# Kernel tuning notes

Hardware: AMD Instinct MI355X
Metric: run time of the kernel (lower is better)

The kernel has to match this reference:

```python
import jax, jax.numpy as jnp
import numpy as np

B, L, D, V, K = 4, 2048, 1024, 32, 4096  # batch, seq, embedding_dim, vq_dim, num_embeddings


def setup_inputs() -> dict:
    key = jax.random.key(0)
    k0, k1, k2, k3 = jax.random.split(key, 4)
    h = jax.random.normal(k0, (B, L, D), jnp.float32)
    attn_mask = jnp.ones((B, L), jnp.float32)
    # proj: Linear(D -> V); proj_inv: Linear(V -> D)
    Wp = jax.random.normal(k1, (V, D), jnp.float32) / np.float32(np.sqrt(D))
    bp = jnp.zeros((V,), jnp.float32)
    Wpi = jax.random.normal(k2, (D, V), jnp.float32) / np.float32(np.sqrt(V))
    bpi = jnp.zeros((D,), jnp.float32)
    # embedding init uniform(-1/K, 1/K)
    emb = jax.random.uniform(k3, (K, V), jnp.float32, -1.0 / K, 1.0 / K)
    return {"h": h, "attn_mask": attn_mask, "Wp": Wp, "bp": bp,
            "Wpi": Wpi, "bpi": bpi, "emb": emb}


def reference(h, attn_mask, Wp, bp, Wpi, bpi, emb, temperature=1.0):
    # project + L2 normalize
    hp = jnp.einsum('bld,vd->blv', h, Wp) + bp            # [B,L,V]
    hp = hp / jnp.linalg.norm(hp, axis=-1, keepdims=True)
    # normalize codebook (in torch this is an in-place .data update)
    emb_n = emb / jnp.linalg.norm(emb, axis=-1, keepdims=True)  # [K,V]
    # squared euclidean distances hp vs codebook
    d = (jnp.sum(hp * hp, axis=-1, keepdims=True)
         + jnp.sum(emb_n * emb_n, axis=-1)
         - 2.0 * jnp.einsum('blv,kv->blk', hp, emb_n))    # [B,L,K]
    A = jax.nn.softmax(-d / temperature, axis=-1)         # [B,L,K]
    code = jnp.argmax(A, axis=-1)                         # [B,L]
    h_vq = jnp.einsum('blk,kv->blv', A, emb_n)            # train mode: A @ embedding
    # masked scatter into zeros is equivalent to masking out unselected positions
    m = (attn_mask == 1)
    quantized = jnp.where(m[..., None], h_vq, jnp.float32(0.0))
    vq_code = jnp.where(m, code, 0).astype(jnp.int32)
    quantized = jnp.einsum('blv,dv->bld', quantized, Wpi) + bpi
    vq_loss = jnp.float32(0.0)
    return quantized, vq_code, vq_loss
```

## Files before the change

kernel.cpp:

```cpp
#include <hip/hip_runtime.h>
#include <hip/hip_bf16.h>
#include <math.h>

#define NTOK 8192
#define DIM  1024
#define VDIM 32
#define KCODES 4096

#define SC 2.8853900817779268f

typedef __attribute__((ext_vector_type(8))) short short8;
typedef __attribute__((ext_vector_type(4))) float f32x4;

#define MFMA16(A,B,C) __builtin_amdgcn_mfma_f32_16x16x32_bf16(A, B, C, 0, 0, 0)

__device__ __forceinline__ unsigned short f2bf(float x) {
    unsigned u = __builtin_bit_cast(unsigned, x);
    u += 0x7FFF + ((u >> 16) & 1);
    return (unsigned short)(u >> 16);
}
__device__ __forceinline__ float bf2f(unsigned short b) {
    unsigned u = ((unsigned)b) << 16;
    return __builtin_bit_cast(float, u);
}
__device__ __forceinline__ float fexp2(float x) {
#if __has_builtin(__builtin_amdgcn_exp2f)
    return __builtin_amdgcn_exp2f(x);
#else
    return __expf(0.6931471805599453f * x);
#endif
}

struct U4 { unsigned x, y, z, w; };

__device__ __forceinline__ void split8(const float* p, short8* H, short8* L) {
    unsigned hh[4], ll[4];
    #pragma unroll
    for (int i = 0; i < 4; ++i) {
        unsigned short a = f2bf(p[2 * i]);
        unsigned short b = f2bf(p[2 * i + 1]);
        hh[i] = (unsigned)a | ((unsigned)b << 16);
        unsigned short la = f2bf(p[2 * i] - bf2f(a));
        unsigned short lb = f2bf(p[2 * i + 1] - bf2f(b));
        ll[i] = (unsigned)la | ((unsigned)lb << 16);
    }
    U4 uh = {hh[0], hh[1], hh[2], hh[3]};
    U4 ul = {ll[0], ll[1], ll[2], ll[3]};
    *H = __builtin_bit_cast(short8, uh);
    *L = __builtin_bit_cast(short8, ul);
}

__device__ __forceinline__ short8 pack8(const float* p) {
    unsigned u[8];
    #pragma unroll
    for (int j = 0; j < 8; ++j) u[j] = __builtin_bit_cast(unsigned, p[j]) + 0x8000u;
    U4 uh;
    uh.x = __builtin_amdgcn_perm(u[1], u[0], 0x07060302);
    uh.y = __builtin_amdgcn_perm(u[3], u[2], 0x07060302);
    uh.z = __builtin_amdgcn_perm(u[5], u[4], 0x07060302);
    uh.w = __builtin_amdgcn_perm(u[7], u[6], 0x07060302);
    return __builtin_bit_cast(short8, uh);
}

#define OFS_E_HI   0
#define OFS_E_LO   131072
#define OFS_ET_HI  262144
#define OFS_WP_HI  393216
#define OFS_WP_LO  425984
#define OFS_WPI_HI 458752
#define OFS_WPI_LO 491520
#define OFS_HP_HI  524288
#define OFS_HP_LO  786432
#define F32_BASE   1048576
#define NSPLIT 8
#define FOFS_HVP 0
#define FOFS_LP  2097152
#define FOFS_AMP 2162688
#define FOFS_AIP 2228224

__global__ __launch_bounds__(256) void k_prep(const float* __restrict__ emb,
                                              const float* __restrict__ Wp,
                                              const float* __restrict__ Wpi,
                                              unsigned short* __restrict__ W,
                                              float* __restrict__ loss_out) {
    __shared__ __align__(16) unsigned short Th[32][72];
    int bid = blockIdx.x, tid = threadIdx.x;
    if (bid < 64) {
        int cb = bid * 64;
        int c = tid >> 2, s = tid & 3;
        const float* src = emb + (size_t)(cb + c) * VDIM + s * 8;
        float4 a = *(const float4*)src;
        float4 b = *(const float4*)(src + 4);
        float ps = a.x*a.x + a.y*a.y + a.z*a.z + a.w*a.w
                 + b.x*b.x + b.y*b.y + b.z*b.z + b.w*b.w;
        ps += __shfl_xor(ps, 1);
        ps += __shfl_xor(ps, 2);
        float inv = 1.0f / sqrtf(ps);
        float vals[8] = {a.x*inv, a.y*inv, a.z*inv, a.w*inv,
                         b.x*inv, b.y*inv, b.z*inv, b.w*inv};
        short8 H, L;
        split8(vals, &H, &L);
        *(short8*)(W + OFS_E_HI + (size_t)(cb + c) * VDIM + s * 8) = H;
        *(short8*)(W + OFS_E_LO + (size_t)(cb + c) * VDIM + s * 8) = L;
        #pragma unroll
        for (int j = 0; j < 8; ++j) Th[s * 8 + j][c] = f2bf(vals[j]);
        __syncthreads();
        int row = tid >> 3, seg = tid & 7;
        *(short8*)(W + OFS_ET_HI + (size_t)row * KCODES + cb + seg * 8) =
            *(const short8*)&Th[row][seg * 8];
        if (bid == 0 && tid == 0) loss_out[0] = 0.0f;
    } else if (bid < 80) {
        int i0 = (bid - 64) * 2048 + tid * 8;
        float4 a = *(const float4*)(Wp + i0);
        float4 b = *(const float4*)(Wp + i0 + 4);
        float vals[8] = {a.x, a.y, a.z, a.w, b.x, b.y, b.z, b.w};
        short8 H, L;
        split8(vals, &H, &L);
        *(short8*)(W + OFS_WP_HI + i0) = H;
        *(short8*)(W + OFS_WP_LO + i0) = L;
    } else {
        int i0 = (bid - 80) * 2048 + tid * 8;
        float4 a = *(const float4*)(Wpi + i0);
        float4 b = *(const float4*)(Wpi + i0 + 4);
        float vals[8] = {a.x, a.y, a.z, a.w, b.x, b.y, b.z, b.w};
        short8 H, L;
        split8(vals, &H, &L);
        *(short8*)(W + OFS_WPI_HI + i0) = H;
        *(short8*)(W + OFS_WPI_LO + i0) = L;
    }
}

__global__ __launch_bounds__(256) void k_proj(const float* __restrict__ h,
                                              const unsigned short* __restrict__ W,
                                              const float* __restrict__ bp,
                                              unsigned short* __restrict__ hp_hi,
                                              unsigned short* __restrict__ hp_lo) {
    __shared__ __align__(16) float red[4][16][36];
    const unsigned short* Wp_hi = W + OFS_WP_HI;
    const unsigned short* Wp_lo = W + OFS_WP_LO;
    int tid = threadIdx.x;
    int w = tid >> 6, l = tid & 63, q = l >> 4, m = l & 15;
    int tok0 = blockIdx.x * 16;
    const f32x4 zero4 = {0.f, 0.f, 0.f, 0.f};
    f32x4 acc0 = zero4, acc1 = zero4;
    const float* hb = h + (size_t)(tok0 + m) * DIM + w * 256 + q * 8;
    const unsigned short* w0h = Wp_hi + (size_t)m * DIM + w * 256 + q * 8;
    const unsigned short* w0l = Wp_lo + (size_t)m * DIM + w * 256 + q * 8;
    const unsigned short* w1h = w0h + (size_t)16 * DIM;
    const unsigned short* w1l = w0l + (size_t)16 * DIM;
    #pragma unroll
    for (int c = 0; c < 8; ++c) {
        float4 a = *(const float4*)(hb + c * 32);
        float4 b = *(const float4*)(hb + c * 32 + 4);
        float va[8] = {a.x, a.y, a.z, a.w, b.x, b.y, b.z, b.w};
        short8 Bh, Bl;
        split8(va, &Bh, &Bl);
        short8 A0h = *(const short8*)(w0h + c * 32);
        short8 A0l = *(const short8*)(w0l + c * 32);
        short8 A1h = *(const short8*)(w1h + c * 32);
        short8 A1l = *(const short8*)(w1l + c * 32);
        acc0 = MFMA16(A0l, Bl, acc0); acc0 = MFMA16(A0l, Bh, acc0);
        acc0 = MFMA16(A0h, Bl, acc0); acc0 = MFMA16(A0h, Bh, acc0);
        acc1 = MFMA16(A1l, Bl, acc1); acc1 = MFMA16(A1l, Bh, acc1);
        acc1 = MFMA16(A1h, Bl, acc1); acc1 = MFMA16(A1h, Bh, acc1);
    }
    *(f32x4*)&red[w][m][4 * q]      = acc0;
    *(f32x4*)&red[w][m][16 + 4 * q] = acc1;
    __syncthreads();
    #pragma unroll
    for (int half = 0; half < 2; ++half) {
        int t = (tid >> 5) + half * 8, v = tid & 31;
        float s = bp[v];
        #pragma unroll
        for (int j = 0; j < 4; ++j) s += red[j][t][v];
        float sq = s * s;
        #pragma unroll
        for (int off = 1; off < 32; off <<= 1) sq += __shfl_xor(sq, off);
        float nv = s * (SC / sqrtf(sq));
        unsigned short hb2 = f2bf(nv);
        size_t idx = (size_t)(tok0 + t) * VDIM + v;
        hp_hi[idx] = hb2;
        hp_lo[idx] = f2bf(nv - bf2f(hb2));
    }
}

__global__ __launch_bounds__(256) void k_vq(const unsigned short* __restrict__ W,
                                            float* __restrict__ hvp,
                                            float* __restrict__ lp,
                                            float* __restrict__ amp,
                                            int* __restrict__ aip) {
    const unsigned short* E_hi  = W + OFS_E_HI;
    const unsigned short* E_lo  = W + OFS_E_LO;
    const unsigned short* Et_hi = W + OFS_ET_HI;
    const unsigned short* hp_hi = W + OFS_HP_HI;
    const unsigned short* hp_lo = W + OFS_HP_LO;

    int tid = threadIdx.x;
    int w = tid >> 6, l = tid & 63, q = l >> 4, m = l & 15;
    int tg = blockIdx.x >> 3, sp = blockIdx.x & 7;
    int tok0 = tg * 64 + w * 16;
    int cb0 = sp * 512;
    int sig = ((m & 12) << 1) | (m & 3);
    const f32x4 zero4 = {0.f, 0.f, 0.f, 0.f};

    size_t hidx = (size_t)(tok0 + m) * VDIM + q * 8;
    short8 hph = *(const short8*)(hp_hi + hidx);
    short8 hpl = *(const short8*)(hp_lo + hidx);

    f32x4 hv0 = zero4, hv1 = zero4;
    float ls = 0.f, am = -1e30f;
    int ai = 0;

    #pragma unroll 2
    for (int c = 0; c < 16; ++c) {
        int cbase = cb0 + c * 32;
        size_t e0 = (size_t)(cbase + sig) * VDIM + q * 8;
        short8 E0h = *(const short8*)(E_hi + e0);
        short8 E0l = *(const short8*)(E_lo + e0);
        short8 E1h = *(const short8*)(E_hi + e0 + 4 * VDIM);
        short8 E1l = *(const short8*)(E_lo + e0 + 4 * VDIM);
        size_t t0 = (size_t)sig * KCODES + cbase + q * 8;
        short8 T0h = *(const short8*)(Et_hi + t0);
        short8 T1h = *(const short8*)(Et_hi + t0 + (size_t)4 * KCODES);

        f32x4 s0 = MFMA16(E0l, hpl, zero4);
        s0 = MFMA16(E0l, hph, s0);
        s0 = MFMA16(E0h, hpl, s0);
        s0 = MFMA16(E0h, hph, s0);
        f32x4 s1 = MFMA16(E1l, hpl, zero4);
        s1 = MFMA16(E1l, hph, s1);
        s1 = MFMA16(E1h, hpl, s1);
        s1 = MFMA16(E1h, hph, s1);

        float p[8];
        int lbase = cbase + 8 * q;
        #pragma unroll
        for (int r = 0; r < 4; ++r) {
            float sv = s0[r];
            if (sv > am) { am = sv; ai = lbase + r; }
            p[r] = fexp2(sv);
            sv = s1[r];
            if (sv > am) { am = sv; ai = lbase + 4 + r; }
            p[4 + r] = fexp2(sv);
        }
        ls += ((p[0] + p[1]) + (p[2] + p[3])) + ((p[4] + p[5]) + (p[6] + p[7]));
        short8 Ph = pack8(p);
        hv0 = MFMA16(T0h, Ph, hv0);
        hv1 = MFMA16(T1h, Ph, hv1);
    }

    #pragma unroll
    for (int off = 16; off <= 32; off <<= 1) {
        ls += __shfl_xor(ls, off);
        float a2 = __shfl_xor(am, off);
        int   i2 = __shfl_xor(ai, off);
        if (a2 > am || (a2 == am && i2 < ai)) { am = a2; ai = i2; }
    }
    size_t gtok = (size_t)sp * NTOK + tok0;
    if (q == 0) {
        lp[gtok + m] = ls; amp[gtok + m] = am; aip[gtok + m] = ai;
    }
    float* dst = hvp + (gtok + m) * VDIM;
    *(f32x4*)(dst + 8 * q)     = hv0;
    *(f32x4*)(dst + 8 * q + 4) = hv1;
}

__global__ __launch_bounds__(256) void k_out(const unsigned short* __restrict__ W,
                                             const float* __restrict__ mask,
                                             const float* __restrict__ bpi,
                                             const float* __restrict__ hvp,
                                             const float* __restrict__ lp,
                                             const float* __restrict__ amp,
                                             const int* __restrict__ aip,
                                             float* __restrict__ out,
                                             float* __restrict__ code_out) {
    __shared__ float invl[16];
    __shared__ __align__(16) unsigned short hvh[16][40];
    __shared__ __align__(16) unsigned short hvl[16][40];
    const unsigned short* Wpi_hi = W + OFS_WPI_HI;
    const unsigned short* Wpi_lo = W + OFS_WPI_LO;
    int tid = threadIdx.x;
    int tok0 = blockIdx.x * 16;
    const f32x4 zero4 = {0.f, 0.f, 0.f, 0.f};

    if (tid < 16) {
        int tk = tok0 + tid;
        float L = 0.f, A = -1e30f;
        int I = 0x7fffffff;
        #pragma unroll
        for (int sp = 0; sp < NSPLIT; ++sp) {
            size_t gi = (size_t)sp * NTOK + tk;
            L += lp[gi];
            float a2 = amp[gi];
            int   i2 = aip[gi];
            if (a2 > A || (a2 == A && i2 < I)) { A = a2; I = i2; }
        }
        bool on = (mask[tk] == 1.0f);
        code_out[tk] = on ? (float)I : 0.0f;
        invl[tid] = on ? (1.0f / L) : 0.0f;
    }
    __syncthreads();
    #pragma unroll
    for (int it = 0; it < 2; ++it) {
        int idx = it * 256 + tid;
        int t = idx >> 5, v = idx & 31;
        float x = 0.f;
        #pragma unroll
        for (int sp = 0; sp < NSPLIT; ++sp)
            x += hvp[((size_t)sp * NTOK + tok0 + t) * VDIM + v];
        x *= invl[t];
        unsigned short hb = f2bf(x);
        hvh[t][v] = hb;
        hvl[t][v] = f2bf(x - bf2f(hb));
    }
    __syncthreads();
    int w = tid >> 6, l = tid & 63, q = l >> 4, m = l & 15;
    short8 gh = *(const short8*)&hvh[m][q * 8];
    short8 gl = *(const short8*)&hvl[m][q * 8];
    #pragma unroll
    for (int dt = 0; dt < 16; ++dt) {
        int dbase = w * 256 + dt * 16;
        short8 Ah = *(const short8*)(Wpi_hi + (size_t)(dbase + m) * VDIM + q * 8);
        short8 Al = *(const short8*)(Wpi_lo + (size_t)(dbase + m) * VDIM + q * 8);
        f32x4 o = MFMA16(Al, gh, zero4);
        o = MFMA16(Ah, gl, o);
        o = MFMA16(Ah, gh, o);
        float4 bias = *(const float4*)(bpi + dbase + 4 * q);
        float4 r0 = make_float4(o[0] + bias.x, o[1] + bias.y,
                                o[2] + bias.z, o[3] + bias.w);
        *(float4*)(out + (size_t)(tok0 + m) * DIM + dbase + 4 * q) = r0;
    }
}

extern "C" void kernel_launch(void* const* d_in, const int* in_sizes, int n_in,
                              void* d_out, int out_size, void* d_ws, size_t ws_size,
                              hipStream_t stream) {
    const float* h    = (const float*)d_in[0];
    const float* mask = (const float*)d_in[1];
    const float* Wp   = (const float*)d_in[2];
    const float* bp   = (const float*)d_in[3];
    const float* Wpi  = (const float*)d_in[4];
    const float* bpi  = (const float*)d_in[5];
    const float* emb  = (const float*)d_in[6];
    float* out = (float*)d_out;

    unsigned short* W = (unsigned short*)d_ws;
    unsigned short* hp_hi = W + OFS_HP_HI;
    unsigned short* hp_lo = W + OFS_HP_LO;
    float* fbase = (float*)(W + F32_BASE);
    float* hvp = fbase + FOFS_HVP;
    float* lpp = fbase + FOFS_LP;
    float* ampp = fbase + FOFS_AMP;
    int*   aipp = (int*)(fbase + FOFS_AIP);

    float* code_out = out + (size_t)NTOK * DIM;
    float* loss_out = code_out + NTOK;

    hipLaunchKernelGGL(k_prep, dim3(96),   dim3(256), 0, stream, emb, Wp, Wpi, W, loss_out);
    hipLaunchKernelGGL(k_proj, dim3(512),  dim3(256), 0, stream, h, W, bp, hp_hi, hp_lo);
    hipLaunchKernelGGL(k_vq,   dim3(1024), dim3(256), 0, stream, W, hvp, lpp, ampp, aipp);
    hipLaunchKernelGGL(k_out,  dim3(512),  dim3(256), 0, stream, W, mask, bpi, hvp, lpp, ampp, aipp, out, code_out);
}
```

Baseline: 151.8 us.

## Stage codebook tiles in swizzled LDS with double buffering and prefetch

The VQ kernel now cooperatively loads 128-code slices of the hi/lo codebook into double-buffered, swizzled shared memory instead of having every wave read them from global memory. The next tile is prefetched into registers while the current one is computed, and the transposed codebook fragment is software-pipelined one chunk ahead. It also drops the lo*lo MFMA term, going from four to three MFMAs per product, and adds an occupancy hint to launch bounds. This costs LDS, a barrier per tile, slightly lower score precision, and an out-of-range prefetch read on the last chunk.

```diff
diff --git a/kernel.cpp b/kernel.cpp
--- a/kernel.cpp
+++ b/kernel.cpp
@@ -60,6 +60,11 @@
     uh.z = __builtin_amdgcn_perm(u[5], u[4], 0x07060302);
     uh.w = __builtin_amdgcn_perm(u[7], u[6], 0x07060302);
     return __builtin_bit_cast(short8, uh);
+}
+
+__device__ __forceinline__ int lsw(int row, int j) {
+    int s = ((row >> 1) ^ (row >> 3)) & 3;
+    return row * 40 + ((j ^ s) * 8);
 }
 
 #define OFS_E_HI   0
@@ -184,11 +189,14 @@
     }
 }
 
-__global__ __launch_bounds__(256) void k_vq(const unsigned short* __restrict__ W,
-                                            float* __restrict__ hvp,
-                                            float* __restrict__ lp,
-                                            float* __restrict__ amp,
-                                            int* __restrict__ aip) {
+__global__ __launch_bounds__(256, 4) void k_vq(const unsigned short* __restrict__ W,
+                                               float* __restrict__ hvp,
+                                               float* __restrict__ lp,
+                                               float* __restrict__ amp,
+                                               int* __restrict__ aip) {
+    __shared__ __align__(16) unsigned short Eh[2][128 * 40];
+    __shared__ __align__(16) unsigned short El[2][128 * 40];
+
     const unsigned short* E_hi  = W + OFS_E_HI;
     const unsigned short* E_lo  = W + OFS_E_LO;
     const unsigned short* Et_hi = W + OFS_ET_HI;
@@ -203,50 +211,93 @@
     int sig = ((m & 12) << 1) | (m & 3);
     const f32x4 zero4 = {0.f, 0.f, 0.f, 0.f};
 
+    int c0s = tid >> 2, j0s = tid & 3;
+    int c1s = (tid + 256) >> 2, j1s = tid & 3;
+    int ld0 = lsw(c0s, j0s), ld1 = lsw(c1s, j1s);
+    size_t g0 = (size_t)c0s * VDIM + j0s * 8;
+    size_t g1 = (size_t)c1s * VDIM + j1s * 8;
+
     size_t hidx = (size_t)(tok0 + m) * VDIM + q * 8;
     short8 hph = *(const short8*)(hp_hi + hidx);
     short8 hpl = *(const short8*)(hp_lo + hidx);
 
+    {
+        size_t tb = (size_t)cb0 * VDIM;
+        short8 a0 = *(const short8*)(E_hi + tb + g0);
+        short8 a1 = *(const short8*)(E_hi + tb + g1);
+        short8 b0 = *(const short8*)(E_lo + tb + g0);
+        short8 b1 = *(const short8*)(E_lo + tb + g1);
+        *(short8*)&Eh[0][ld0] = a0;
+        *(short8*)&Eh[0][ld1] = a1;
+        *(short8*)&El[0][ld0] = b0;
+        *(short8*)&El[0][ld1] = b1;
+    }
+    __syncthreads();
+
     f32x4 hv0 = zero4, hv1 = zero4;
     float ls = 0.f, am = -1e30f;
     int ai = 0;
 
-    #pragma unroll 2
-    for (int c = 0; c < 16; ++c) {
-        int cbase = cb0 + c * 32;
-        size_t e0 = (size_t)(cbase + sig) * VDIM + q * 8;
-        short8 E0h = *(const short8*)(E_hi + e0);
-        short8 E0l = *(const short8*)(E_lo + e0);
-        short8 E1h = *(const short8*)(E_hi + e0 + 4 * VDIM);
-        short8 E1l = *(const short8*)(E_lo + e0 + 4 * VDIM);
-        size_t t0 = (size_t)sig * KCODES + cbase + q * 8;
-        short8 T0h = *(const short8*)(Et_hi + t0);
-        short8 T1h = *(const short8*)(Et_hi + t0 + (size_t)4 * KCODES);
-
-        f32x4 s0 = MFMA16(E0l, hpl, zero4);
-        s0 = MFMA16(E0l, hph, s0);
-        s0 = MFMA16(E0h, hpl, s0);
-        s0 = MFMA16(E0h, hph, s0);
-        f32x4 s1 = MFMA16(E1l, hpl, zero4);
-        s1 = MFMA16(E1l, hph, s1);
-        s1 = MFMA16(E1h, hpl, s1);
-        s1 = MFMA16(E1h, hph, s1);
-
-        float p[8];
-        int lbase = cbase + 8 * q;
-        #pragma unroll
-        for (int r = 0; r < 4; ++r) {
-            float sv = s0[r];
-            if (sv > am) { am = sv; ai = lbase + r; }
-            p[r] = fexp2(sv);
-            sv = s1[r];
-            if (sv > am) { am = sv; ai = lbase + 4 + r; }
-            p[4 + r] = fexp2(sv);
+    size_t tA = (size_t)sig * KCODES + cb0 + q * 8;
+    short8 T0h = *(const short8*)(Et_hi + tA);
+    short8 T1h = *(const short8*)(Et_hi + tA + (size_t)4 * KCODES);
+
+    #pragma unroll 1
+    for (int t = 0; t < 4; ++t) {
+        int buf = t & 1;
+        short8 sa0, sa1, sb0, sb1;
+        if (t < 3) {
+            size_t tb = (size_t)(cb0 + (t + 1) * 128) * VDIM;
+            sa0 = *(const short8*)(E_hi + tb + g0);
+            sa1 = *(const short8*)(E_hi + tb + g1);
+            sb0 = *(const short8*)(E_lo + tb + g0);
+            sb1 = *(const short8*)(E_lo + tb + g1);
         }
-        ls += ((p[0] + p[1]) + (p[2] + p[3])) + ((p[4] + p[5]) + (p[6] + p[7]));
-        short8 Ph = pack8(p);
-        hv0 = MFMA16(T0h, Ph, hv0);
-        hv1 = MFMA16(T1h, Ph, hv1);
+        #pragma unroll
+        for (int cc = 0; cc < 4; ++cc) {
+            int gch = t * 4 + cc;
+            int cbase = cb0 + gch * 32;
+            size_t tN = (size_t)sig * KCODES + (cbase + 32) + q * 8;
+            short8 nT0h = *(const short8*)(Et_hi + tN);
+            short8 nT1h = *(const short8*)(Et_hi + tN + (size_t)4 * KCODES);
+            int r0 = cc * 32 + sig;
+            short8 E0h = *(const short8*)&Eh[buf][lsw(r0, q)];
+            short8 E0l = *(const short8*)&El[buf][lsw(r0, q)];
+            short8 E1h = *(const short8*)&Eh[buf][lsw(r0 + 4, q)];
+            short8 E1l = *(const short8*)&El[buf][lsw(r0 + 4, q)];
+
+            f32x4 s0 = MFMA16(E0h, hpl, zero4);
+            s0 = MFMA16(E0l, hph, s0);
+            s0 = MFMA16(E0h, hph, s0);
+            f32x4 s1 = MFMA16(E1h, hpl, zero4);
+            s1 = MFMA16(E1l, hph, s1);
+            s1 = MFMA16(E1h, hph, s1);
+
+            float p[8];
+            int lbase = cbase + 8 * q;
+            #pragma unroll
+            for (int r = 0; r < 4; ++r) {
+                float sv = s0[r];
+                if (sv > am) { am = sv; ai = lbase + r; }
+                p[r] = fexp2(sv);
+                sv = s1[r];
+                if (sv > am) { am = sv; ai = lbase + 4 + r; }
+                p[4 + r] = fexp2(sv);
+            }
+            ls += ((p[0] + p[1]) + (p[2] + p[3])) + ((p[4] + p[5]) + (p[6] + p[7]));
+            short8 Ph = pack8(p);
+            hv0 = MFMA16(T0h, Ph, hv0);
+            hv1 = MFMA16(T1h, Ph, hv1);
+            T0h = nT0h; T1h = nT1h;
+        }
+        if (t < 3) {
+            int nb = buf ^ 1;
+            *(short8*)&Eh[nb][ld0] = sa0;
+            *(short8*)&Eh[nb][ld1] = sa1;
+            *(short8*)&El[nb][ld0] = sb0;
+            *(short8*)&El[nb][ld1] = sb1;
+            __syncthreads();
+        }
     }
 
     #pragma unroll
```

After: 148.8 us. -2.0%, faster.
